# Kernel optimization log

Measured on AMD Instinct MI355X. Metric: run time of the kernel, lower is better.

The kernel has to match this reference:

```python
import math
import jax, jax.numpy as jnp
import numpy as np

B, L, D = 16, 2048, 64  # batch, seq len (m == n, self-attention), head dim
C = 30                   # ProbSparse sampling factor c


def setup_inputs() -> dict:
    key = jax.random.key(0)
    kq, kk, kv = jax.random.split(key, 3)
    Q = jax.random.normal(kq, (B, L, D), dtype=jnp.float32)
    K = jax.random.normal(kk, (B, L, D), dtype=jnp.float32)
    V = jax.random.normal(kv, (B, L, D), dtype=jnp.float32)
    return {"Q": Q, "K": K, "V": V, "seed": 0}


def reference(Q, K, V, seed):
    b, m, d = Q.shape
    n = K.shape[1]
    u = int(C * math.log(m))              # number of active queries
    U = min(int(m * math.log(n)), n)      # number of sampled keys (clamped to n)
    inv_sqrt_d = 1.0 / math.sqrt(d)

    rngs = jax.random.split(jax.random.key(seed), b)

    def _each_sample(Qb, Kb, Vb, r):
        # random sample of U key rows without replacement
        idx = jax.random.choice(r, n, shape=(U,), replace=False)
        Kbar = Kb[idx]                                # [U, d]
        Sbar = jnp.matmul(Qb, Kbar.T)                 # [m, U]
        M = jnp.max(Sbar, axis=1) - jnp.mean(Sbar, axis=1)  # sparsity measure [m]
        _, I = jax.lax.top_k(M, u)                    # active query indices [u]
        Qbar = Qb[I]                                  # [u, d]
        A = jax.nn.softmax(jnp.matmul(Qbar, Kb.T) * inv_sqrt_d, axis=-1)  # [u, n]
        S1 = jnp.matmul(A, Vb)                        # [u, d]
        # literal source: fill with mean(V, axis=1, keepdims=True) -> (n,1) broadcast (m==n)
        S = jnp.broadcast_to(jnp.mean(Vb, axis=1, keepdims=True), (m, d))
        return S.at[I].set(S1)

    return jax.vmap(_each_sample)(Q, K, V, rngs)
```

## Files before the change

### kernel.cpp

```cpp
#include <hip/hip_runtime.h>

#define NB 16
#define NN 2048
#define DH 64
#define NSEL 228
#define KS 4
#define CHUNK (NN / KS)
#define RS 4
#define EPSBAND 2.0e-3f
#define MAXB 32

using s16x8 = __attribute__((ext_vector_type(8))) short;
using f32x16 = __attribute__((ext_vector_type(16))) float;

static __device__ __forceinline__ unsigned short f2bf(float x) {
  unsigned int u = __float_as_uint(x);
  u += 0x7fffu + ((u >> 16) & 1u);
  return (unsigned short)(u >> 16);
}
static __device__ __forceinline__ float bf2f(unsigned short h) {
  return __uint_as_float(((unsigned int)h) << 16);
}
static __device__ __forceinline__ unsigned int enc(float f) {
  unsigned int u = __float_as_uint(f);
  return (u & 0x80000000u) ? ~u : (u | 0x80000000u);
}
static __device__ __forceinline__ float dec(unsigned int k) {
  return (k & 0x80000000u) ? __uint_as_float(k & 0x7fffffffu)
                           : __uint_as_float(~k);
}

__global__ __launch_bounds__(256) void conv_fused(const float* __restrict__ K,
                                                  const float* __restrict__ V,
                                                  unsigned short* __restrict__ Khi,
                                                  unsigned short* __restrict__ Klo,
                                                  unsigned short* __restrict__ VThi,
                                                  unsigned short* __restrict__ VTlo,
                                                  float* __restrict__ Kpart) {
  __shared__ __align__(16) float T[64][65];
  const int b = blockIdx.y, ch = blockIdx.x;
  const int tid = threadIdx.x;
  const int r = tid >> 2;
  const int c0 = (tid & 3) * 16;

  if (blockIdx.z == 0) {
    const size_t off = ((size_t)b * NN + ch * 64 + r) * DH + c0;
    const float* src = K + off;
    float v[16];
    #pragma unroll
    for (int f = 0; f < 4; ++f) {
      float4 x = *(const float4*)(src + f * 4);
      v[f * 4 + 0] = x.x; v[f * 4 + 1] = x.y;
      v[f * 4 + 2] = x.z; v[f * 4 + 3] = x.w;
      T[r][c0 + f * 4 + 0] = x.x;
      T[r][c0 + f * 4 + 1] = x.y;
      T[r][c0 + f * 4 + 2] = x.z;
      T[r][c0 + f * 4 + 3] = x.w;
    }
    #pragma unroll
    for (int half = 0; half < 2; ++half) {
      union { unsigned short u[8]; s16x8 s; } H, L;
      #pragma unroll
      for (int j = 0; j < 8; ++j) {
        const float x = v[half * 8 + j];
        const unsigned short hh = f2bf(x);
        H.u[j] = hh;
        L.u[j] = f2bf(x - bf2f(hh));
      }
      *(s16x8*)(Khi + off + half * 8) = H.s;
      *(s16x8*)(Klo + off + half * 8) = L.s;
    }
    __syncthreads();
    if (tid < 64) {
      float s = 0.f;
      #pragma unroll 8
      for (int rr = 0; rr < 64; ++rr) s += T[rr][tid];
      Kpart[((size_t)b * 32 + ch) * 64 + tid] = s;
    }
  } else {
    const float* src = V + ((size_t)b * NN + ch * 64 + r) * DH + c0;
    #pragma unroll
    for (int f = 0; f < 4; ++f) {
      float4 x = *(const float4*)(src + f * 4);
      T[r][c0 + f * 4 + 0] = x.x;
      T[r][c0 + f * 4 + 1] = x.y;
      T[r][c0 + f * 4 + 2] = x.z;
      T[r][c0 + f * 4 + 3] = x.w;
    }
    __syncthreads();
    const int d = tid >> 2;
    const int j0 = (tid & 3) * 16;
    unsigned short* oh = VThi + ((size_t)b * DH + d) * NN + ch * 64 + j0;
    unsigned short* ol = VTlo + ((size_t)b * DH + d) * NN + ch * 64 + j0;
    #pragma unroll
    for (int half = 0; half < 2; ++half) {
      union { unsigned short u[8]; s16x8 s; } H, L;
      #pragma unroll
      for (int c = 0; c < 8; ++c) {
        const float x = T[j0 + half * 8 + c][d];
        const unsigned short hh = f2bf(x);
        H.u[c] = hh;
        L.u[c] = f2bf(x - bf2f(hh));
      }
      *(s16x8*)(oh + half * 8) = H.s;
      *(s16x8*)(ol + half * 8) = L.s;
    }
  }
}

__global__ __launch_bounds__(256, 4) void rowstat_mfma(const float* __restrict__ Q,
                                                       const unsigned short* __restrict__ Khi,
                                                       const unsigned short* __restrict__ Klo,
                                                       float* __restrict__ Mmax) {
  __shared__ __align__(16) unsigned short KHs[128 * 64];
  __shared__ __align__(16) unsigned short KLs[128 * 64];
  const int b = blockIdx.y, cz = blockIdx.z;
  const int qbase = blockIdx.x * 128;
  const int tid = threadIdx.x;
  const int w = tid >> 6, lane = tid & 63;
  const int l31 = lane & 31, hi5 = lane >> 5;

  s16x8 qh[4], ql[4];
  {
    const float* qrow = Q + ((size_t)b * NN + qbase + w * 32 + l31) * DH;
    #pragma unroll
    for (int ks = 0; ks < 4; ++ks) {
      const int d0 = ks * 16 + hi5 * 8;
      float4 x = *(const float4*)(qrow + d0);
      float4 y = *(const float4*)(qrow + d0 + 4);
      float v[8] = {x.x, x.y, x.z, x.w, y.x, y.y, y.z, y.w};
      union { unsigned short u[8]; s16x8 s; } H, L;
      #pragma unroll
      for (int j = 0; j < 8; ++j) {
        unsigned short h = f2bf(v[j]);
        H.u[j] = h;
        L.u[j] = f2bf(v[j] - bf2f(h));
      }
      qh[ks] = H.s;
      ql[ks] = L.s;
    }
  }

  const size_t kbase = ((size_t)b * NN + cz * (NN / RS)) * DH;
  f32x16 vmax;
  #pragma unroll
  for (int i = 0; i < 16; ++i) vmax[i] = -3.0e38f;

  const int sr = tid >> 1;
  const int sh = tid & 1;

  for (int stage = 0; stage < NN / RS / 128; ++stage) {
    __syncthreads();
    {
      const size_t g = kbase + (size_t)(stage * 128 + sr) * DH + sh * 32;
      const unsigned short* gh = Khi + g;
      const unsigned short* gl = Klo + g;
      #pragma unroll
      for (int c = 0; c < 4; ++c) {
        s16x8 hv = *(const s16x8*)(gh + c * 8);
        s16x8 lv = *(const s16x8*)(gl + c * 8);
        const int chn = (sh * 4 + c) ^ (sr & 7);
        *(s16x8*)&KHs[(sr * 8 + chn) * 8] = hv;
        *(s16x8*)&KLs[(sr * 8 + chn) * 8] = lv;
      }
    }
    __syncthreads();

    #pragma unroll
    for (int ksub = 0; ksub < 4; ++ksub) {
      const int kr = ksub * 32 + l31;
      f32x16 acc;
      #pragma unroll
      for (int i = 0; i < 16; ++i) acc[i] = 0.f;
      #pragma unroll
      for (int ks = 0; ks < 4; ++ks) {
        const int chn = (ks * 2 + hi5) ^ (kr & 7);
        s16x8 ah = *(const s16x8*)&KHs[(kr * 8 + chn) * 8];
        s16x8 al = *(const s16x8*)&KLs[(kr * 8 + chn) * 8];
        acc = __builtin_amdgcn_mfma_f32_32x32x16_bf16(ah, qh[ks], acc, 0, 0, 0);
        acc = __builtin_amdgcn_mfma_f32_32x32x16_bf16(al, qh[ks], acc, 0, 0, 0);
        acc = __builtin_amdgcn_mfma_f32_32x32x16_bf16(ah, ql[ks], acc, 0, 0, 0);
      }
      #pragma unroll
      for (int i = 0; i < 16; ++i) vmax[i] = fmaxf(vmax[i], acc[i]);
    }
  }

  float m = vmax[0];
  #pragma unroll
  for (int i = 1; i < 16; ++i) m = fmaxf(m, vmax[i]);
  m = fmaxf(m, __shfl_xor(m, 32));
  if (lane < 32)
    Mmax[((size_t)cz * NB + b) * NN + qbase + w * 32 + lane] = m;
}

__global__ __launch_bounds__(256) void mstat_kernel(const float* __restrict__ Q,
                                                    const float* __restrict__ Mmax,
                                                    const float* __restrict__ Kpart,
                                                    unsigned int* __restrict__ keysW,
                                                    float* __restrict__ meanv) {
  __shared__ float Ksl[64];
  const int b = blockIdx.y;
  const int seg = blockIdx.x;
  const int tid = threadIdx.x;
  if (tid < 64) {
    float s = 0.f;
    #pragma unroll
    for (int c = 0; c < 32; ++c) s += Kpart[((size_t)b * 32 + c) * 64 + tid];
    Ksl[tid] = s;
  }
  __syncthreads();
  const int i = seg * 256 + tid;
  float mv = -3.0e38f;
  #pragma unroll
  for (int cz = 0; cz < RS; ++cz)
    mv = fmaxf(mv, Mmax[((size_t)cz * NB + b) * NN + i]);
  const float* qrow = Q + ((size_t)b * NN + i) * DH;
  float s = 0.f;
  #pragma unroll
  for (int d4 = 0; d4 < 16; ++d4) {
    float4 qv = *(const float4*)(qrow + d4 * 4);
    s = fmaf(qv.x, Ksl[d4 * 4 + 0], s);
    s = fmaf(qv.y, Ksl[d4 * 4 + 1], s);
    s = fmaf(qv.z, Ksl[d4 * 4 + 2], s);
    s = fmaf(qv.w, Ksl[d4 * 4 + 3], s);
  }
  const float mean = s * (1.0f / NN);
  meanv[(size_t)b * NN + i] = mean;
  keysW[(size_t)b * NN + i] = enc(mv - mean);
}

static __device__ unsigned int radix_thresh(const unsigned int* kreg, int lane,
                                            int wid, int* red) {
  unsigned int v = 0u;
  for (int bit = 31; bit >= 0; --bit) {
    const unsigned int cand = v | (1u << bit);
    int c = 0;
    #pragma unroll
    for (int f = 0; f < 8; ++f) c += (kreg[f] >= cand) ? 1 : 0;
    #pragma unroll
    for (int off = 1; off < 64; off <<= 1) c += __shfl_xor(c, off);
    if (lane == 0) red[wid] = c;
    __syncthreads();
    if (red[0] + red[1] + red[2] + red[3] >= NSEL) v = cand;
    __syncthreads();
  }
  return v;
}

__global__ __launch_bounds__(256) void radix1_kernel(const unsigned int* __restrict__ keysW,
                                                     int* __restrict__ Band,
                                                     int* __restrict__ nband) {
  __shared__ int red[4];
  __shared__ int cntS;
  const int b = blockIdx.x;
  const int tid = threadIdx.x;
  const int lane = tid & 63, wid = tid >> 6;
  const int base = tid * 8;

  unsigned int kreg[8];
  #pragma unroll
  for (int f = 0; f < 8; ++f) kreg[f] = keysW[(size_t)b * NN + base + f];
  if (tid == 0) cntS = 0;
  __syncthreads();

  const unsigned int v1 = radix_thresh(kreg, lane, wid, red);
  const float vf = dec(v1);

  #pragma unroll
  for (int f = 0; f < 8; ++f) {
    if (fabsf(dec(kreg[f]) - vf) <= EPSBAND) {
      int p = atomicAdd(&cntS, 1);
      Band[(size_t)b * NN + p] = base + f;
    }
  }
  __syncthreads();
  if (tid == 0) nband[b] = cntS;
}

__global__ __launch_bounds__(256) void recheck_kernel(const float* __restrict__ Q,
                                                      const float* __restrict__ K,
                                                      const int* __restrict__ Band,
                                                      const int* __restrict__ nband,
                                                      const float* __restrict__ meanv,
                                                      unsigned int* __restrict__ keysW) {
  __shared__ float qsh[64];
  __shared__ float fred[4];
  const int b = blockIdx.y;
  const int nb_ = nband[b];
  const int tid = threadIdx.x;
  const int lane = tid & 63, wid = tid >> 6;

  for (int n = blockIdx.x; n < nb_; n += MAXB) {
    const int row = Band[(size_t)b * NN + n];
    __syncthreads();
    if (tid < 64) qsh[tid] = Q[((size_t)b * NN + row) * DH + tid];
    __syncthreads();
    float lmax = -3.0e38f;
    for (int j = tid; j < NN; j += 256) {
      const float* krow = K + ((size_t)b * NN + j) * DH;
      float s = 0.f;
      #pragma unroll
      for (int d4 = 0; d4 < 16; ++d4) {
        float4 kv = *(const float4*)(krow + d4 * 4);
        s = fmaf(kv.x, qsh[d4 * 4 + 0], s);
        s = fmaf(kv.y, qsh[d4 * 4 + 1], s);
        s = fmaf(kv.z, qsh[d4 * 4 + 2], s);
        s = fmaf(kv.w, qsh[d4 * 4 + 3], s);
      }
      lmax = fmaxf(lmax, s);
    }
    #pragma unroll
    for (int off = 1; off < 64; off <<= 1)
      lmax = fmaxf(lmax, __shfl_xor(lmax, off));
    if (lane == 0) fred[wid] = lmax;
    __syncthreads();
    if (tid == 0) {
      const float mx = fmaxf(fmaxf(fred[0], fred[1]), fmaxf(fred[2], fred[3]));
      keysW[(size_t)b * NN + row] = enc(mx - meanv[(size_t)b * NN + row]);
    }
  }
}

__global__ __launch_bounds__(256) void radix2_kernel(const unsigned int* __restrict__ keysW,
                                                     int* __restrict__ Isel,
                                                     int* __restrict__ pos) {
  __shared__ int red[4];
  const int b = blockIdx.x;
  const int tid = threadIdx.x;
  const int lane = tid & 63, wid = tid >> 6;
  const int base = tid * 8;

  unsigned int kreg[8];
  #pragma unroll
  for (int f = 0; f < 8; ++f) kreg[f] = keysW[(size_t)b * NN + base + f];
  __syncthreads();

  const unsigned int v2 = radix_thresh(kreg, lane, wid, red);

  int flg[8];
  int cnt = 0;
  #pragma unroll
  for (int f = 0; f < 8; ++f) { flg[f] = (kreg[f] > v2) ? 1 : 0; cnt += flg[f]; }
  int scan = cnt;
  #pragma unroll
  for (int off = 1; off < 64; off <<= 1) {
    const int t = __shfl_up(scan, off);
    if (lane >= off) scan += t;
  }
  if (lane == 63) red[wid] = scan;
  __syncthreads();
  int wbase = 0;
  for (int ww = 0; ww < wid; ++ww) wbase += red[ww];
  const int cg = red[0] + red[1] + red[2] + red[3];
  int p = wbase + scan - cnt;
  #pragma unroll
  for (int f = 0; f < 8; ++f) {
    if (flg[f]) {
      Isel[b * NSEL + p] = base + f;
      pos[(size_t)b * NN + base + f] = p;
      ++p;
    } else {
      pos[(size_t)b * NN + base + f] = -1;
    }
  }
  __syncthreads();

  const int need = NSEL - cg;
  cnt = 0;
  #pragma unroll
  for (int f = 0; f < 8; ++f) { flg[f] = (kreg[f] == v2) ? 1 : 0; cnt += flg[f]; }
  scan = cnt;
  #pragma unroll
  for (int off = 1; off < 64; off <<= 1) {
    const int t = __shfl_up(scan, off);
    if (lane >= off) scan += t;
  }
  if (lane == 63) red[wid] = scan;
  __syncthreads();
  wbase = 0;
  for (int ww = 0; ww < wid; ++ww) wbase += red[ww];
  p = wbase + scan - cnt;
  #pragma unroll
  for (int f = 0; f < 8; ++f) {
    if (flg[f]) {
      if (p < need) {
        Isel[b * NSEL + cg + p] = base + f;
        pos[(size_t)b * NN + base + f] = cg + p;
      }
      ++p;
    }
  }
}

__global__ __launch_bounds__(256, 2) void attn_mfma(const float* __restrict__ Q,
                                                    const unsigned short* __restrict__ Khi,
                                                    const unsigned short* __restrict__ Klo,
                                                    const unsigned short* __restrict__ VThi,
                                                    const unsigned short* __restrict__ VTlo,
                                                    const int* __restrict__ Isel,
                                                    float* __restrict__ Pm,
                                                    float* __restrict__ Pl,
                                                    float* __restrict__ Po) {
  __shared__ float wmax[4][32];
  __shared__ float wl[4][32];
  __shared__ __align__(16) float Opart[4][32][68];
  const int b = blockIdx.z, kc = blockIdx.y, g = blockIdx.x;
  const int tid = threadIdx.x, w = tid >> 6, lane = tid & 63;
  const int l31 = lane & 31, h = lane >> 5;

  const int lq = g * 32 + l31;
  const int qidx = (lq < NSEL) ? Isel[b * NSEL + lq] : Isel[b * NSEL];
  s16x8 qbh[4], qbl[4];
  {
    const float* qr = Q + ((size_t)b * NN + qidx) * DH;
    #pragma unroll
    for (int s = 0; s < 4; ++s) {
      const int d0 = s * 16 + h * 8;
      float4 x = *(const float4*)(qr + d0);
      float4 y = *(const float4*)(qr + d0 + 4);
      float v[8] = {x.x, x.y, x.z, x.w, y.x, y.y, y.z, y.w};
      union { unsigned short u[8]; s16x8 s8; } H, L;
      #pragma unroll
      for (int j = 0; j < 8; ++j) {
        const unsigned short hh = f2bf(v[j]);
        H.u[j] = hh;
        L.u[j] = f2bf(v[j] - bf2f(hh));
      }
      qbh[s] = H.s8;
      qbl[s] = L.s8;
    }
  }

  const size_t krow0 = (size_t)b * NN + kc * CHUNK + w * 128;
  f32x16 p[4];
  #pragma unroll
  for (int t = 0; t < 4; ++t) {
    const unsigned short* kh = Khi + (krow0 + t * 32 + l31) * DH + h * 8;
    const unsigned short* kl = Klo + (krow0 + t * 32 + l31) * DH + h * 8;
    f32x16 acc;
    #pragma unroll
    for (int i = 0; i < 16; ++i) acc[i] = 0.f;
    #pragma unroll
    for (int s = 0; s < 4; ++s) {
      const s16x8 ah = *(const s16x8*)(kh + s * 16);
      const s16x8 al = *(const s16x8*)(kl + s * 16);
      acc = __builtin_amdgcn_mfma_f32_32x32x16_bf16(ah, qbh[s], acc, 0, 0, 0);
      acc = __builtin_amdgcn_mfma_f32_32x32x16_bf16(al, qbh[s], acc, 0, 0, 0);
      acc = __builtin_amdgcn_mfma_f32_32x32x16_bf16(ah, qbl[s], acc, 0, 0, 0);
    }
    p[t] = acc;
  }

  float rmax = p[0][0];
  #pragma unroll
  for (int t = 0; t < 4; ++t)
    #pragma unroll
    for (int i = 0; i < 16; ++i) rmax = fmaxf(rmax, p[t][i]);
  rmax = fmaxf(rmax, __shfl_xor(rmax, 32));
  if (lane < 32) wmax[w][lane] = rmax;
  __syncthreads();
  const float gmax = fmaxf(fmaxf(wmax[0][l31], wmax[1][l31]),
                           fmaxf(wmax[2][l31], wmax[3][l31]));
  const float m = gmax * 0.125f;

  float lsum = 0.f;
  #pragma unroll
  for (int t = 0; t < 4; ++t)
    #pragma unroll
    for (int i = 0; i < 16; ++i) {
      const float e = __expf(fmaf(p[t][i], 0.125f, -m));
      p[t][i] = e;
      lsum += e;
    }
  lsum += __shfl_xor(lsum, 32);
  if (lane < 32) wl[w][lane] = lsum;

  f32x16 oacc[2];
  #pragma unroll
  for (int i = 0; i < 16; ++i) { oacc[0][i] = 0.f; oacc[1][i] = 0.f; }

  #pragma unroll
  for (int s = 0; s < 8; ++s) {
    const int t = s >> 1, kb = s & 1;
    float pr[8];
    #pragma unroll
    for (int j = 0; j < 8; ++j) pr[j] = p[t][kb * 8 + j];
    unsigned int ah[4], al[4];
    #pragma unroll
    for (int pi = 0; pi < 4; ++pi) {
      const unsigned short h0 = f2bf(pr[pi * 2]);
      const unsigned short h1 = f2bf(pr[pi * 2 + 1]);
      ah[pi] = (unsigned int)h0 | ((unsigned int)h1 << 16);
      al[pi] = (unsigned int)f2bf(pr[pi * 2] - bf2f(h0)) |
               ((unsigned int)f2bf(pr[pi * 2 + 1] - bf2f(h1)) << 16);
    }
    unsigned int sh_[4], sl_[4];
    #pragma unroll
    for (int pi = 0; pi < 4; ++pi) {
      sh_[pi] = (unsigned int)__shfl_xor((int)ah[pi], 32);
      sl_[pi] = (unsigned int)__shfl_xor((int)al[pi], 32);
    }
    union { int4 i4; s16x8 s8; } BH, BL;
    if (h == 0) {
      BH.i4 = make_int4((int)ah[0], (int)ah[1], (int)sh_[0], (int)sh_[1]);
      BL.i4 = make_int4((int)al[0], (int)al[1], (int)sl_[0], (int)sl_[1]);
    } else {
      BH.i4 = make_int4((int)sh_[2], (int)sh_[3], (int)ah[2], (int)ah[3]);
      BL.i4 = make_int4((int)sl_[2], (int)sl_[3], (int)al[2], (int)al[3]);
    }
    const size_t koff = (size_t)kc * CHUNK + w * 128 + s * 16 + h * 8;
    #pragma unroll
    for (int dt = 0; dt < 2; ++dt) {
      const size_t vrow = ((size_t)b * DH + dt * 32 + l31) * NN + koff;
      const s16x8 av = *(const s16x8*)(VThi + vrow);
      const s16x8 avl = *(const s16x8*)(VTlo + vrow);
      oacc[dt] = __builtin_amdgcn_mfma_f32_32x32x16_bf16(av, BH.s8, oacc[dt], 0, 0, 0);
      oacc[dt] = __builtin_amdgcn_mfma_f32_32x32x16_bf16(av, BL.s8, oacc[dt], 0, 0, 0);
      oacc[dt] = __builtin_amdgcn_mfma_f32_32x32x16_bf16(avl, BH.s8, oacc[dt], 0, 0, 0);
    }
  }

  #pragma unroll
  for (int dt = 0; dt < 2; ++dt)
    #pragma unroll
    for (int rg = 0; rg < 4; ++rg) {
      const int d0 = dt * 32 + rg * 8 + h * 4;
      float4 vv;
      vv.x = oacc[dt][rg * 4 + 0];
      vv.y = oacc[dt][rg * 4 + 1];
      vv.z = oacc[dt][rg * 4 + 2];
      vv.w = oacc[dt][rg * 4 + 3];
      *(float4*)&Opart[w][l31][d0] = vv;
    }
  __syncthreads();

  const int q = tid >> 3, dg = (tid & 7) * 8;
  float4 s0, s1;
  s0.x = s0.y = s0.z = s0.w = 0.f;
  s1.x = s1.y = s1.z = s1.w = 0.f;
  #pragma unroll
  for (int ww = 0; ww < 4; ++ww) {
    const float4 a = *(const float4*)&Opart[ww][q][dg];
    const float4 c = *(const float4*)&Opart[ww][q][dg + 4];
    s0.x += a.x; s0.y += a.y; s0.z += a.z; s0.w += a.w;
    s1.x += c.x; s1.y += c.y; s1.z += c.z; s1.w += c.w;
  }
  const int lq2 = g * 32 + q;
  if (lq2 < NSEL) {
    const size_t row = ((size_t)b * NSEL + lq2) * KS + kc;
    *(float4*)(Po + row * 64 + dg) = s0;
    *(float4*)(Po + row * 64 + dg + 4) = s1;
    if (dg == 0) {
      const float gm2 = fmaxf(fmaxf(wmax[0][q], wmax[1][q]),
                              fmaxf(wmax[2][q], wmax[3][q]));
      Pm[row] = gm2 * 0.125f;
      Pl[row] = wl[0][q] + wl[1][q] + wl[2][q] + wl[3][q];
    }
  }
}

__global__ __launch_bounds__(256) void fill_combine(const float* __restrict__ V,
                                                    const int* __restrict__ pos,
                                                    const float* __restrict__ Pm,
                                                    const float* __restrict__ Pl,
                                                    const float* __restrict__ Po,
                                                    float* __restrict__ out) {
  const size_t row = (size_t)blockIdx.x * 4 + (threadIdx.x >> 6);
  const int lane = threadIdx.x & 63;
  const int p = pos[row];
  if (p < 0) {
    float x = V[row * DH + lane];
    #pragma unroll
    for (int off = 1; off < 64; off <<= 1) x += __shfl_xor(x, off);
    out[row * DH + lane] = x * (1.0f / DH);
  } else {
    const int b = (int)(row / NN);
    const size_t base = ((size_t)b * NSEL + p) * KS;
    float pm[KS];
    float gm = -3.0e38f;
    #pragma unroll
    for (int c = 0; c < KS; ++c) { pm[c] = Pm[base + c]; gm = fmaxf(gm, pm[c]); }
    float L = 0.f, od = 0.f;
    #pragma unroll
    for (int c = 0; c < KS; ++c) {
      const float e = __expf(pm[c] - gm);
      L += Pl[base + c] * e;
      od += Po[(base + c) * 64 + lane] * e;
    }
    out[row * DH + lane] = od / L;
  }
}

extern "C" void kernel_launch(void* const* d_in, const int* in_sizes, int n_in,
                              void* d_out, int out_size, void* d_ws, size_t ws_size,
                              hipStream_t stream) {
  const float* Q = (const float*)d_in[0];
  const float* K = (const float*)d_in[1];
  const float* V = (const float*)d_in[2];
  float* out = (float*)d_out;

  float* Mmax = (float*)d_ws;
  float* Kpart = Mmax + (size_t)RS * NB * NN;
  unsigned int* keysW = (unsigned int*)(Kpart + (size_t)NB * 32 * 64);
  float* meanv = (float*)(keysW + (size_t)NB * NN);
  int* Band = (int*)(meanv + (size_t)NB * NN);
  int* nband = Band + (size_t)NB * NN;
  int* Isel = nband + 16;
  int* posA = Isel + NB * NSEL;
  float* Pm = (float*)(posA + (size_t)NB * NN);
  float* Pl = Pm + (size_t)NB * NSEL * KS;
  float* Po = Pl + (size_t)NB * NSEL * KS;
  unsigned short* Khi = (unsigned short*)(Po + (size_t)NB * NSEL * KS * 64);
  unsigned short* Klo = Khi + (size_t)NB * NN * DH;
  unsigned short* VThi = Klo + (size_t)NB * NN * DH;
  unsigned short* VTlo = VThi + (size_t)NB * NN * DH;

  conv_fused<<<dim3(NN / 64, NB, 2), 256, 0, stream>>>(K, V, Khi, Klo, VThi,
                                                       VTlo, Kpart);
  rowstat_mfma<<<dim3(NN / 128, NB, RS), 256, 0, stream>>>(Q, Khi, Klo, Mmax);
  mstat_kernel<<<dim3(8, NB), 256, 0, stream>>>(Q, Mmax, Kpart, keysW, meanv);
  radix1_kernel<<<dim3(NB), 256, 0, stream>>>(keysW, Band, nband);
  recheck_kernel<<<dim3(MAXB, NB), 256, 0, stream>>>(Q, K, Band, nband, meanv, keysW);
  radix2_kernel<<<dim3(NB), 256, 0, stream>>>(keysW, Isel, posA);
  attn_mfma<<<dim3(8, KS, NB), 256, 0, stream>>>(Q, Khi, Klo, VThi, VTlo, Isel,
                                                 Pm, Pl, Po);
  fill_combine<<<dim3(NB * NN / 4), 256, 0, stream>>>(V, posA, Pm, Pl, Po, out);
}
```

Baseline: 222.1 us.

## Fuse row-stat with mean/key computation and merge selection kernels into one

The split-K rowstat kernel (RS=4 partial maxima) is folded into a single pass over all keys that also computes the mean and the encoded sparsity key, which removes the Mmax buffer and the mstat kernel. The radix1, recheck and radix2 kernels become one per-batch kernel that keeps keys and the band list in shared memory. This cuts five launches down to two and avoids global round trips. The costs are less parallelism: the rowstat grid shrinks fourfold (256 blocks), and the band recheck now runs serially in just 16 blocks instead of being spread over 32×16 blocks.

```diff
diff --git a/kernel.cpp b/kernel.cpp
--- a/kernel.cpp
+++ b/kernel.cpp
@@ -6,9 +6,7 @@
 #define NSEL 228
 #define KS 4
 #define CHUNK (NN / KS)
-#define RS 4
 #define EPSBAND 2.0e-3f
-#define MAXB 32
 
 using s16x8 = __attribute__((ext_vector_type(8))) short;
 using f32x16 = __attribute__((ext_vector_type(16))) float;
@@ -108,17 +106,27 @@
   }
 }
 
-__global__ __launch_bounds__(256, 4) void rowstat_mfma(const float* __restrict__ Q,
+__global__ __launch_bounds__(256, 1) void rowstat_keys(const float* __restrict__ Q,
                                                        const unsigned short* __restrict__ Khi,
                                                        const unsigned short* __restrict__ Klo,
-                                                       float* __restrict__ Mmax) {
+                                                       const float* __restrict__ Kpart,
+                                                       unsigned int* __restrict__ keysW,
+                                                       float* __restrict__ meanv) {
   __shared__ __align__(16) unsigned short KHs[128 * 64];
   __shared__ __align__(16) unsigned short KLs[128 * 64];
-  const int b = blockIdx.y, cz = blockIdx.z;
+  __shared__ float Ksl[64];
+  const int b = blockIdx.y;
   const int qbase = blockIdx.x * 128;
   const int tid = threadIdx.x;
   const int w = tid >> 6, lane = tid & 63;
   const int l31 = lane & 31, hi5 = lane >> 5;
+
+  if (tid < 64) {
+    float s = 0.f;
+    #pragma unroll
+    for (int c = 0; c < 32; ++c) s += Kpart[((size_t)b * 32 + c) * 64 + tid];
+    Ksl[tid] = s;
+  }
 
   s16x8 qh[4], ql[4];
   {
@@ -141,7 +149,7 @@
     }
   }
 
-  const size_t kbase = ((size_t)b * NN + cz * (NN / RS)) * DH;
+  const size_t kbase = (size_t)b * NN * DH;
   f32x16 vmax;
   #pragma unroll
   for (int i = 0; i < 16; ++i) vmax[i] = -3.0e38f;
@@ -149,7 +157,7 @@
   const int sr = tid >> 1;
   const int sh = tid & 1;
 
-  for (int stage = 0; stage < NN / RS / 128; ++stage) {
+  for (int stage = 0; stage < NN / 128; ++stage) {
     __syncthreads();
     {
       const size_t g = kbase + (size_t)(stage * 128 + sr) * DH + sh * 32;
@@ -190,44 +198,23 @@
   #pragma unroll
   for (int i = 1; i < 16; ++i) m = fmaxf(m, vmax[i]);
   m = fmaxf(m, __shfl_xor(m, 32));
-  if (lane < 32)
-    Mmax[((size_t)cz * NB + b) * NN + qbase + w * 32 + lane] = m;
-}
-
-__global__ __launch_bounds__(256) void mstat_kernel(const float* __restrict__ Q,
-                                                    const float* __restrict__ Mmax,
-                                                    const float* __restrict__ Kpart,
-                                                    unsigned int* __restrict__ keysW,
-                                                    float* __restrict__ meanv) {
-  __shared__ float Ksl[64];
-  const int b = blockIdx.y;
-  const int seg = blockIdx.x;
-  const int tid = threadIdx.x;
-  if (tid < 64) {
-    float s = 0.f;
-    #pragma unroll
-    for (int c = 0; c < 32; ++c) s += Kpart[((size_t)b * 32 + c) * 64 + tid];
-    Ksl[tid] = s;
-  }
-  __syncthreads();
-  const int i = seg * 256 + tid;
-  float mv = -3.0e38f;
-  #pragma unroll
-  for (int cz = 0; cz < RS; ++cz)
-    mv = fmaxf(mv, Mmax[((size_t)cz * NB + b) * NN + i]);
-  const float* qrow = Q + ((size_t)b * NN + i) * DH;
-  float s = 0.f;
-  #pragma unroll
-  for (int d4 = 0; d4 < 16; ++d4) {
-    float4 qv = *(const float4*)(qrow + d4 * 4);
-    s = fmaf(qv.x, Ksl[d4 * 4 + 0], s);
-    s = fmaf(qv.y, Ksl[d4 * 4 + 1], s);
-    s = fmaf(qv.z, Ksl[d4 * 4 + 2], s);
-    s = fmaf(qv.w, Ksl[d4 * 4 + 3], s);
-  }
-  const float mean = s * (1.0f / NN);
-  meanv[(size_t)b * NN + i] = mean;
-  keysW[(size_t)b * NN + i] = enc(mv - mean);
+
+  if (lane < 32) {
+    const int row = qbase + w * 32 + lane;
+    const float* qr = Q + ((size_t)b * NN + row) * DH;
+    float dot = 0.f;
+    #pragma unroll
+    for (int d4 = 0; d4 < 16; ++d4) {
+      float4 qv = *(const float4*)(qr + d4 * 4);
+      dot = fmaf(qv.x, Ksl[d4 * 4 + 0], dot);
+      dot = fmaf(qv.y, Ksl[d4 * 4 + 1], dot);
+      dot = fmaf(qv.z, Ksl[d4 * 4 + 2], dot);
+      dot = fmaf(qv.w, Ksl[d4 * 4 + 3], dot);
+    }
+    const float mean = dot * (1.0f / NN);
+    meanv[(size_t)b * NN + row] = mean;
+    keysW[(size_t)b * NN + row] = enc(m - mean);
+  }
 }
 
 static __device__ unsigned int radix_thresh(const unsigned int* kreg, int lane,
@@ -248,9 +235,16 @@
   return v;
 }
 
-__global__ __launch_bounds__(256) void radix1_kernel(const unsigned int* __restrict__ keysW,
-                                                     int* __restrict__ Band,
-                                                     int* __restrict__ nband) {
+__global__ __launch_bounds__(256) void select_fused(const float* __restrict__ Q,
+                                                    const float* __restrict__ K,
+                                                    const unsigned int* __restrict__ keysW,
+                                                    const float* __restrict__ meanv,
+                                                    int* __restrict__ Isel,
+                                                    int* __restrict__ posA) {
+  __shared__ unsigned int skeys[NN];
+  __shared__ int blist[NN];
+  __shared__ float qsh[64];
+  __shared__ float fred[4];
   __shared__ int red[4];
   __shared__ int cntS;
   const int b = blockIdx.x;
@@ -260,39 +254,27 @@
 
   unsigned int kreg[8];
   #pragma unroll
-  for (int f = 0; f < 8; ++f) kreg[f] = keysW[(size_t)b * NN + base + f];
+  for (int f = 0; f < 8; ++f) {
+    kreg[f] = keysW[(size_t)b * NN + base + f];
+    skeys[base + f] = kreg[f];
+  }
   if (tid == 0) cntS = 0;
   __syncthreads();
 
   const unsigned int v1 = radix_thresh(kreg, lane, wid, red);
   const float vf = dec(v1);
-
   #pragma unroll
   for (int f = 0; f < 8; ++f) {
     if (fabsf(dec(kreg[f]) - vf) <= EPSBAND) {
       int p = atomicAdd(&cntS, 1);
-      Band[(size_t)b * NN + p] = base + f;
-    }
-  }
-  __syncthreads();
-  if (tid == 0) nband[b] = cntS;
-}
-
-__global__ __launch_bounds__(256) void recheck_kernel(const float* __restrict__ Q,
-                                                      const float* __restrict__ K,
-                                                      const int* __restrict__ Band,
-                                                      const int* __restrict__ nband,
-                                                      const float* __restrict__ meanv,
-                                                      unsigned int* __restrict__ keysW) {
-  __shared__ float qsh[64];
-  __shared__ float fred[4];
-  const int b = blockIdx.y;
-  const int nb_ = nband[b];
-  const int tid = threadIdx.x;
-  const int lane = tid & 63, wid = tid >> 6;
-
-  for (int n = blockIdx.x; n < nb_; n += MAXB) {
-    const int row = Band[(size_t)b * NN + n];
+      blist[p] = base + f;
+    }
+  }
+  __syncthreads();
+  const int nb_ = cntS;
+
+  for (int n = 0; n < nb_; ++n) {
+    const int row = blist[n];
     __syncthreads();
     if (tid < 64) qsh[tid] = Q[((size_t)b * NN + row) * DH + tid];
     __syncthreads();
@@ -317,24 +299,12 @@
     __syncthreads();
     if (tid == 0) {
       const float mx = fmaxf(fmaxf(fred[0], fred[1]), fmaxf(fred[2], fred[3]));
-      keysW[(size_t)b * NN + row] = enc(mx - meanv[(size_t)b * NN + row]);
-    }
-  }
-}
-
-__global__ __launch_bounds__(256) void radix2_kernel(const unsigned int* __restrict__ keysW,
-                                                     int* __restrict__ Isel,
-                                                     int* __restrict__ pos) {
-  __shared__ int red[4];
-  const int b = blockIdx.x;
-  const int tid = threadIdx.x;
-  const int lane = tid & 63, wid = tid >> 6;
-  const int base = tid * 8;
-
-  unsigned int kreg[8];
-  #pragma unroll
-  for (int f = 0; f < 8; ++f) kreg[f] = keysW[(size_t)b * NN + base + f];
-  __syncthreads();
+      skeys[row] = enc(mx - meanv[(size_t)b * NN + row]);
+    }
+  }
+  __syncthreads();
+  #pragma unroll
+  for (int f = 0; f < 8; ++f) kreg[f] = skeys[base + f];
 
   const unsigned int v2 = radix_thresh(kreg, lane, wid, red);
 
@@ -358,10 +328,10 @@
   for (int f = 0; f < 8; ++f) {
     if (flg[f]) {
       Isel[b * NSEL + p] = base + f;
-      pos[(size_t)b * NN + base + f] = p;
+      posA[(size_t)b * NN + base + f] = p;
       ++p;
     } else {
-      pos[(size_t)b * NN + base + f] = -1;
+      posA[(size_t)b * NN + base + f] = -1;
     }
   }
   __syncthreads();
@@ -386,7 +356,7 @@
     if (flg[f]) {
       if (p < need) {
         Isel[b * NSEL + cg + p] = base + f;
-        pos[(size_t)b * NN + base + f] = cg + p;
+        posA[(size_t)b * NN + base + f] = cg + p;
       }
       ++p;
     }
@@ -600,13 +570,10 @@
   const float* V = (const float*)d_in[2];
   float* out = (float*)d_out;
 
-  float* Mmax = (float*)d_ws;
-  float* Kpart = Mmax + (size_t)RS * NB * NN;
+  float* Kpart = (float*)d_ws;
   unsigned int* keysW = (unsigned int*)(Kpart + (size_t)NB * 32 * 64);
   float* meanv = (float*)(keysW + (size_t)NB * NN);
-  int* Band = (int*)(meanv + (size_t)NB * NN);
-  int* nband = Band + (size_t)NB * NN;
-  int* Isel = nband + 16;
+  int* Isel = (int*)(meanv + (size_t)NB * NN);
   int* posA = Isel + NB * NSEL;
   float* Pm = (float*)(posA + (size_t)NB * NN);
   float* Pl = Pm + (size_t)NB * NSEL * KS;
@@ -618,11 +585,9 @@
 
   conv_fused<<<dim3(NN / 64, NB, 2), 256, 0, stream>>>(K, V, Khi, Klo, VThi,
                                                        VTlo, Kpart);
-  rowstat_mfma<<<dim3(NN / 128, NB, RS), 256, 0, stream>>>(Q, Khi, Klo, Mmax);
-  mstat_kernel<<<dim3(8, NB), 256, 0, stream>>>(Q, Mmax, Kpart, keysW, meanv);
-  radix1_kernel<<<dim3(NB), 256, 0, stream>>>(keysW, Band, nband);
-  recheck_kernel<<<dim3(MAXB, NB), 256, 0, stream>>>(Q, K, Band, nband, meanv, keysW);
-  radix2_kernel<<<dim3(NB), 256, 0, stream>>>(keysW, Isel, posA);
+  rowstat_keys<<<dim3(NN / 128, NB), 256, 0, stream>>>(Q, Khi, Klo, Kpart,
+                                                       keysW, meanv);
+  select_fused<<<dim3(NB), 256, 0, stream>>>(Q, K, keysW, meanv, Isel, posA);
   attn_mfma<<<dim3(8, KS, NB), 256, 0, stream>>>(Q, Khi, Klo, VThi, VTlo, Isel,
                                                  Pm, Pl, Po);
   fill_combine<<<dim3(NB * NN / 4), 256, 0, stream>>>(V, posA, Pm, Pl, Po, out);
```

After: 213.7 us. -3.8%, faster.
